# Optimization experiments

Hardware: AMD Instinct MI355X
Metric: run time of the kernel (lower is better)

## Reference

```python
import jax, jax.numpy as jnp
import numpy as np

N, IN_FEATS, OUT_FEATS = 8192, 512, 256


def setup_inputs() -> dict:
    key = jax.random.key(0)
    k1, k2, k3, k4 = jax.random.split(key, 4)
    feature_mat = jax.random.normal(k1, (N, IN_FEATS), dtype=jnp.float32)
    # Xavier-uniform style init for W and W2
    limW = float(np.sqrt(6.0 / (IN_FEATS + OUT_FEATS)))
    W = jax.random.uniform(k2, (IN_FEATS, OUT_FEATS), minval=-limW, maxval=limW, dtype=jnp.float32)
    limW2 = float(np.sqrt(6.0 / (2 * OUT_FEATS + 1)))
    W2 = jax.random.uniform(k3, (2 * OUT_FEATS, 1), minval=-limW2, maxval=limW2, dtype=jnp.float32)
    adj_mat = jax.random.randint(k4, (N, N), 0, 2, dtype=jnp.int32)
    return {"feature_mat": feature_mat, "W": W, "W2": W2, "adj_mat": adj_mat}


def reference(feature_mat, W, W2, adj_mat):
    out_feats = W.shape[1]
    Wh = feature_mat @ W                      # [N, F']
    Wh1 = Wh @ W2[:out_feats, :]              # [N, 1]
    Wh2 = Wh @ W2[out_feats:, :]              # [N, 1]
    e = Wh1 + Wh2.T                           # [N, N] broadcast add
    e = jnp.where(e > 0, e, 0.2 * e)          # leaky_relu(0.2)
    # NOTE: original masks with ZERO (not -inf) before softmax — faithful.
    e = jnp.where(adj_mat > 0, e, jnp.zeros((), dtype=e.dtype))
    attention = jax.nn.softmax(e, axis=1)     # row softmax over all N
    h_prime = attention @ Wh                  # [N, F']
    return jax.nn.relu(h_prime)
```

## Files before the change

### kernel.cpp

```cpp
#include <hip/hip_runtime.h>
#include <cstdint>
#include <cstddef>

#define NR 8192
#define FOUT 256
#define KIN 512
#define KSPLIT 4
#define JCHUNK (NR / KSPLIT)
#define BKJ 64
#define NSTEP (JCHUNK / BKJ)
#define IROWS 128

typedef __attribute__((ext_vector_type(8))) short bf16x8;
typedef __attribute__((ext_vector_type(4))) float f32x4;

__device__ __forceinline__ unsigned f2bf(float x) {
  unsigned u = __float_as_uint(x);
  u += 0x7fffu + ((u >> 16) & 1u);
  return u >> 16;
}
__device__ __forceinline__ float bf2f(unsigned h) {
  return __uint_as_float(h << 16);
}
__device__ __forceinline__ unsigned fkey(float x) {
  unsigned u = __float_as_uint(x);
  return (u & 0x80000000u) ? ~u : (u | 0x80000000u);
}
__device__ __forceinline__ float fkey_dec(unsigned k) {
  return __uint_as_float((k & 0x80000000u) ? (k ^ 0x80000000u) : ~k);
}

#define GLDS(g, l)                                                            \
  __builtin_amdgcn_global_load_lds(                                           \
      (const __attribute__((address_space(1))) unsigned int*)(g),             \
      (__attribute__((address_space(3))) unsigned int*)(l), 16, 0, 0)

__global__ __launch_bounds__(256) void k0_prep(const float* __restrict__ W,
                                               const float* __restrict__ W2,
                                               float* __restrict__ w1,
                                               float* __restrict__ w2,
                                               char* __restrict__ WTbf,
                                               unsigned* __restrict__ maxkey) {
  if (blockIdx.x == 0 && threadIdx.x == 0) *maxkey = 0u;
  int wv = threadIdx.x >> 6, lane = threadIdx.x & 63;
  int k = blockIdx.x * 4 + wv;
  int f4 = lane * 4;
  float4 wr = *(const float4*)(W + (size_t)k * FOUT + f4);
  float4 a = *(const float4*)(W2 + f4);
  float4 b = *(const float4*)(W2 + FOUT + f4);
  float d1 = wr.x * a.x + wr.y * a.y + wr.z * a.z + wr.w * a.w;
  float d2 = wr.x * b.x + wr.y * b.y + wr.z * b.z + wr.w * b.w;
#pragma unroll
  for (int off = 32; off; off >>= 1) {
    d1 += __shfl_xor(d1, off);
    d2 += __shfl_xor(d2, off);
  }
  if (lane == 0) {
    w1[k] = d1;
    w2[k] = d2;
  }
  int kt = k >> 5, kl = k & 31;
  float wv4[4] = {wr.x, wr.y, wr.z, wr.w};
#pragma unroll
  for (int ff = 0; ff < 4; ++ff) {
    int f = f4 + ff;
    size_t addr = (size_t)kt * 16384 + (f >> 4) * 1024 +
                  (((f & 15) | (((kl >> 3) & 3) << 4)) * 16) + (kl & 7) * 2;
    *(unsigned short*)(WTbf + addr) = (unsigned short)f2bf(wv4[ff]);
  }
}

__global__ __launch_bounds__(256) void k2_fused(
    const float* __restrict__ X, const char* __restrict__ WTbf,
    const float* __restrict__ w1, const float* __restrict__ w2,
    char* __restrict__ WhTf, float* __restrict__ Wh1, float* __restrict__ Wh2,
    unsigned* __restrict__ maxkey) {
  __shared__ char smem[2 * 18432 + 4096];
  char* buf0 = smem;
  char* buf1 = smem + 18432;
  char* wlds = smem + 2 * 18432;
  int t = threadIdx.x, wv = t >> 6, lane = t & 63;
  int jb = blockIdx.x * 32;
  int jr = t >> 3, koff = (t & 7) * 4;
  int cA = (jr & 15) | (((koff >> 3) & 3) << 4);
  int swA = cA ^ (((cA >> 4) & 3) << 2);
  int aoff = (jr >> 4) * 1024 + swA * 16 + ((koff & 4) << 1);
  int slotR = lane ^ (((lane >> 4) & 3) << 2);
  const float* xrow = X + (size_t)(jb + jr) * KIN + koff;

  {
    float2 a_ = *(const float2*)(w1 + t * 2);
    float2 b_ = *(const float2*)(w2 + t * 2);
    *(float2*)(wlds + t * 8) = a_;
    *(float2*)(wlds + 2048 + t * 8) = b_;
  }
  __syncthreads();

  float4 st0, st1, st2, st3;
  float d1 = 0.f, d2 = 0.f;
  f32x4 acc[2][4];
#pragma unroll
  for (int a = 0; a < 2; ++a)
#pragma unroll
    for (int b = 0; b < 4; ++b) acc[a][b] = (f32x4){0.f, 0.f, 0.f, 0.f};

#define K2_GLB(KT, BUFW)                                                      \
  do {                                                                        \
    const char* gs_ = WTbf + ((size_t)(KT) << 14) + (wv << 12) + lane * 16;   \
    char* ld_ = (BUFW) + 2048 + (wv << 12);                                   \
    GLDS(gs_, ld_);                                                           \
    GLDS(gs_ + 1024, ld_ + 1024);                                             \
    GLDS(gs_ + 2048, ld_ + 2048);                                             \
    GLDS(gs_ + 3072, ld_ + 3072);                                             \
  } while (0)

#define K2_LDX(KT, ST) (ST) = *(const float4*)(xrow + (KT) * 32)

#define K2_AGEN(ST, BUFW, SNUM)                                               \
  do {                                                                        \
    uint2 a_;                                                                 \
    a_.x = f2bf((ST).x) | (f2bf((ST).y) << 16);                               \
    a_.y = f2bf((ST).z) | (f2bf((ST).w) << 16);                               \
    *(uint2*)((BUFW) + aoff) = a_;                                            \
    float4 wa_ = *(const float4*)(wlds + ((SNUM)*32 + koff) * 4);             \
    float4 wb_ = *(const float4*)(wlds + 2048 + ((SNUM)*32 + koff) * 4);      \
    d1 += (ST).x * wa_.x + (ST).y * wa_.y + (ST).z * wa_.z + (ST).w * wa_.w;  \
    d2 += (ST).x * wb_.x + (ST).y * wb_.y + (ST).z * wb_.z + (ST).w * wb_.w;  \
  } while (0)

#define K2_ITER(S, BUFR, BUFW, STC, STF)                                      \
  do {                                                                        \
    int s_ = (S);                                                             \
    if (s_ + 1 < 16) K2_GLB(s_ + 1, BUFW);                                    \
    K2_LDX((s_ + 3 < 16) ? s_ + 3 : 15, STF);                                 \
    if (s_ + 1 < 16) K2_AGEN(STC, BUFW, s_ + 1);                              \
    bf16x8 a0 = *(const bf16x8*)((BUFR) + slotR * 16);                        \
    bf16x8 a1 = *(const bf16x8*)((BUFR) + 1024 + slotR * 16);                 \
    bf16x8 b0 = *(const bf16x8*)((BUFR) + 2048 + (wv * 4 + 0) * 1024 + lane * 16); \
    bf16x8 b1 = *(const bf16x8*)((BUFR) + 2048 + (wv * 4 + 1) * 1024 + lane * 16); \
    bf16x8 b2 = *(const bf16x8*)((BUFR) + 2048 + (wv * 4 + 2) * 1024 + lane * 16); \
    bf16x8 b3 = *(const bf16x8*)((BUFR) + 2048 + (wv * 4 + 3) * 1024 + lane * 16); \
    acc[0][0] = __builtin_amdgcn_mfma_f32_16x16x32_bf16(a0, b0, acc[0][0], 0, 0, 0); \
    acc[0][1] = __builtin_amdgcn_mfma_f32_16x16x32_bf16(a0, b1, acc[0][1], 0, 0, 0); \
    acc[0][2] = __builtin_amdgcn_mfma_f32_16x16x32_bf16(a0, b2, acc[0][2], 0, 0, 0); \
    acc[0][3] = __builtin_amdgcn_mfma_f32_16x16x32_bf16(a0, b3, acc[0][3], 0, 0, 0); \
    acc[1][0] = __builtin_amdgcn_mfma_f32_16x16x32_bf16(a1, b0, acc[1][0], 0, 0, 0); \
    acc[1][1] = __builtin_amdgcn_mfma_f32_16x16x32_bf16(a1, b1, acc[1][1], 0, 0, 0); \
    acc[1][2] = __builtin_amdgcn_mfma_f32_16x16x32_bf16(a1, b2, acc[1][2], 0, 0, 0); \
    acc[1][3] = __builtin_amdgcn_mfma_f32_16x16x32_bf16(a1, b3, acc[1][3], 0, 0, 0); \
    __builtin_amdgcn_sched_barrier(0);                                        \
    asm volatile("s_waitcnt vmcnt(1)");                                       \
    asm volatile("s_waitcnt lgkmcnt(0)");                                     \
    __builtin_amdgcn_s_barrier();                                             \
    __builtin_amdgcn_sched_barrier(0);                                        \
  } while (0)

  K2_GLB(0, buf0);
  K2_LDX(0, st0);
  K2_LDX(1, st1);
  K2_LDX(2, st2);
  K2_AGEN(st0, buf0, 0);
  __builtin_amdgcn_sched_barrier(0);
  asm volatile("s_waitcnt vmcnt(2)");
  asm volatile("s_waitcnt lgkmcnt(0)");
  __builtin_amdgcn_s_barrier();
  __builtin_amdgcn_sched_barrier(0);

  for (int s4 = 0; s4 < 16; s4 += 4) {
    K2_ITER(s4 + 0, buf0, buf1, st1, st3);
    K2_ITER(s4 + 1, buf1, buf0, st2, st0);
    K2_ITER(s4 + 2, buf0, buf1, st3, st1);
    K2_ITER(s4 + 3, buf1, buf0, st0, st2);
  }
#undef K2_ITER
#undef K2_AGEN
#undef K2_LDX
#undef K2_GLB

  int q = lane >> 4;
#pragma unroll
  for (int mi = 0; mi < 2; ++mi)
#pragma unroll
    for (int nn = 0; nn < 4; ++nn) {
      int u2 = wv * 4 + nn;
      int cell = (lane & 15) | ((((mi * 2) + (q >> 1)) & 3) << 4);
      uint2 v;
      v.x = f2bf(acc[mi][nn].x) | (f2bf(acc[mi][nn].y) << 16);
      v.y = f2bf(acc[mi][nn].z) | (f2bf(acc[mi][nn].w) << 16);
      *(uint2*)(buf0 + 2048 + u2 * 1024 + cell * 16 + ((q & 1) << 3)) = v;
    }
  __syncthreads();
  char* wb = WhTf + (size_t)blockIdx.x * 16384;
#pragma unroll
  for (int q2 = 0; q2 < 4; ++q2) {
    uint4 v = *(const uint4*)(buf0 + 2048 + q2 * 4096 + t * 16);
    *(uint4*)(wb + q2 * 4096 + t * 16) = v;
  }

  d1 += __shfl_xor(d1, 1);
  d1 += __shfl_xor(d1, 2);
  d1 += __shfl_xor(d1, 4);
  d2 += __shfl_xor(d2, 1);
  d2 += __shfl_xor(d2, 2);
  d2 += __shfl_xor(d2, 4);
  if ((t & 7) == 0) {
    Wh1[jb + jr] = d1;
    Wh2[jb + jr] = d2;
  }
  float mx = d2;
#pragma unroll
  for (int off = 32; off >= 8; off >>= 1) mx = fmaxf(mx, __shfl_xor(mx, off));
  __shared__ float red[4];
  if (lane == 0) red[wv] = mx;
  __syncthreads();
  if (t == 0) {
    float bm = fmaxf(fmaxf(red[0], red[1]), fmaxf(red[2], red[3]));
    atomicMax(maxkey, fkey(bm));
  }
}

__device__ __forceinline__ uint2 hv4(int4 aq, float4 wq, float wh1, float m,
                                     float enm, float& z) {
  float s0 = wh1 + wq.x, s1 = wh1 + wq.y, s2 = wh1 + wq.z, s3 = wh1 + wq.w;
  s0 = s0 > 0.f ? s0 : 0.2f * s0;
  s1 = s1 > 0.f ? s1 : 0.2f * s1;
  s2 = s2 > 0.f ? s2 : 0.2f * s2;
  s3 = s3 > 0.f ? s3 : 0.2f * s3;
  float w0 = aq.x > 0 ? __expf(s0 - m) : enm;
  float w1 = aq.y > 0 ? __expf(s1 - m) : enm;
  float w2 = aq.z > 0 ? __expf(s2 - m) : enm;
  float w3 = aq.w > 0 ? __expf(s3 - m) : enm;
  unsigned h0 = f2bf(w0), h1 = f2bf(w1), h2 = f2bf(w2), h3 = f2bf(w3);
  z += bf2f(h0) + bf2f(h1) + bf2f(h2) + bf2f(h3);
  uint2 r;
  r.x = h0 | (h1 << 16);
  r.y = h2 | (h3 << 16);
  return r;
}
__device__ __forceinline__ uint4 hv8(int4 a0, int4 a1, float4 w0, float4 w1,
                                     float wh1, float m, float enm, float& z) {
  uint2 r0 = hv4(a0, w0, wh1, m, enm, z);
  uint2 r1 = hv4(a1, w1, wh1, m, enm, z);
  return (uint4){r0.x, r0.y, r1.x, r1.y};
}

__global__ __launch_bounds__(1024, 4) void k3_attn(
    const int* __restrict__ adj, const char* __restrict__ WhTf,
    const float* __restrict__ Wh1, const float* __restrict__ Wh2,
    const unsigned* __restrict__ maxptr, float* __restrict__ PVp,
    float* __restrict__ Zp) {
  __shared__ char smem[40960];
  char* abuf0 = smem;
  char* abuf1 = smem + 16384;
  char* wlds = smem + 32768;
  int t = threadIdx.x, wv = t >> 6, lane = t & 63;
  int kc = blockIdx.x & 3;
  int ib = blockIdx.x >> 2;
  int ibase = ib * IROWS;
  int jbch = kc * JCHUNK;
  int r0 = t >> 3;
  int j8 = (t & 7) * 8;
  int iglob = ibase + r0;
  float maxwh2 = fkey_dec(*maxptr);
  float wh1 = Wh1[iglob];
  float m = fmaxf(0.f, wh1 + maxwh2);
  float enm = __expf(-m);
  int unitA = (r0 >> 4) * 2 + (j8 >> 5);
  int cA = (r0 & 15) | (((j8 & 31) >> 3) << 4);
  int swA = cA ^ (((cA >> 4) & 3) << 2);
  int aoff = unitA * 1024 + swA * 16;
  int slotR = lane ^ (((lane >> 4) & 3) << 2);
  const int* adjrow = adj + ((size_t)iglob << 13) + jbch + j8;
  const char* bbase = WhTf + ((size_t)(kc * 64) << 14) + (size_t)wv * 1024 +
                      (size_t)lane * 16;
  const char* wl = wlds + j8 * 4;

  *(float2*)(wlds + t * 8) = *(const float2*)(Wh2 + jbch + t * 2);
  __syncthreads();

  bf16x8 bA0, bA1, bB0, bB1;
  int4 st0_a, st0_b, st1_a, st1_b;
  f32x4 acc[8];
#pragma unroll
  for (int a = 0; a < 8; ++a) acc[a] = (f32x4){0.f, 0.f, 0.f, 0.f};
  float zacc = 0.f;

#define K3_LDB(S, B0, B1)                                                     \
  do {                                                                        \
    int sc_ = (S) < NSTEP ? (S) : NSTEP - 1;                                  \
    const char* bp_ = bbase + (size_t)(2 * sc_) * 16384;                      \
    B0 = *(const bf16x8*)(bp_);                                               \
    B1 = *(const bf16x8*)(bp_ + 16384);                                       \
  } while (0)

#define K3_LDA(S, ST)                                                         \
  do {                                                                        \
    int sc_ = (S) < NSTEP ? (S) : NSTEP - 1;                                  \
    ST##_a = *(const int4*)(adjrow + sc_ * BKJ);                              \
    ST##_b = *(const int4*)(adjrow + sc_ * BKJ + 4);                          \
  } while (0)

#define K3_ITER(S, AR, AW, BC0, BC1, BF0, BF1, STC, DO_HV)                    \
  do {                                                                        \
    int s_ = (S);                                                             \
    K3_LDB(s_ + 1, BF0, BF1);                                                 \
    if (DO_HV) {                                                              \
      float4 wq0_ = *(const float4*)(wl + (s_ + 1) * 256);                    \
      float4 wq1_ = *(const float4*)(wl + (s_ + 1) * 256 + 16);               \
      uint4 a_ = hv8(STC##_a, STC##_b, wq0_, wq1_, wh1, m, enm, zacc);        \
      *(uint4*)((AW) + aoff) = a_;                                            \
    }                                                                         \
    K3_LDA(s_ + 3, STC);                                                      \
    _Pragma("unroll")                                                         \
    for (int rf_ = 0; rf_ < 8; ++rf_) {                                       \
      bf16x8 ak0_ = *(const bf16x8*)((AR) + (rf_ * 2 + 0) * 1024 + slotR * 16); \
      bf16x8 ak1_ = *(const bf16x8*)((AR) + (rf_ * 2 + 1) * 1024 + slotR * 16); \
      acc[rf_] = __builtin_amdgcn_mfma_f32_16x16x32_bf16(ak0_, BC0, acc[rf_], 0, 0, 0); \
      acc[rf_] = __builtin_amdgcn_mfma_f32_16x16x32_bf16(ak1_, BC1, acc[rf_], 0, 0, 0); \
    }                                                                         \
    __builtin_amdgcn_sched_barrier(0);                                        \
    asm volatile("s_waitcnt lgkmcnt(0)" ::: "memory");                        \
    __builtin_amdgcn_s_barrier();                                             \
    __builtin_amdgcn_sched_barrier(0);                                        \
  } while (0)

  K3_LDB(0, bA0, bA1);
  int4 adj0a = *(const int4*)(adjrow);
  int4 adj0b = *(const int4*)(adjrow + 4);
  K3_LDA(1, st1);
  K3_LDA(2, st0);
  {
    float4 wq0 = *(const float4*)(wl);
    float4 wq1 = *(const float4*)(wl + 16);
    uint4 a0 = hv8(adj0a, adj0b, wq0, wq1, wh1, m, enm, zacc);
    *(uint4*)(abuf0 + aoff) = a0;
  }
  __builtin_amdgcn_sched_barrier(0);
  asm volatile("s_waitcnt lgkmcnt(0)" ::: "memory");
  __builtin_amdgcn_s_barrier();
  __builtin_amdgcn_sched_barrier(0);

  for (int s2 = 0; s2 < NSTEP - 2; s2 += 2) {
    K3_ITER(s2 + 0, abuf0, abuf1, bA0, bA1, bB0, bB1, st1, 1);
    K3_ITER(s2 + 1, abuf1, abuf0, bB0, bB1, bA0, bA1, st0, 1);
  }
  K3_ITER(NSTEP - 2, abuf0, abuf1, bA0, bA1, bB0, bB1, st1, 1);
  K3_ITER(NSTEP - 1, abuf1, abuf0, bB0, bB1, bA0, bA1, st0, 0);
#undef K3_ITER
#undef K3_LDA
#undef K3_LDB

  zacc += __shfl_xor(zacc, 1);
  zacc += __shfl_xor(zacc, 2);
  zacc += __shfl_xor(zacc, 4);
  if ((t & 7) == 0) Zp[(size_t)kc * NR + iglob] = zacc;
#pragma unroll
  for (int rf = 0; rf < 8; ++rf) {
    int f = wv * 16 + (lane & 15);
    int row0 = ibase + rf * 16 + ((lane >> 4) << 2);
    size_t base = ((size_t)kc * NR + row0) * FOUT + f;
    PVp[base + 0 * FOUT] = acc[rf].x;
    PVp[base + 1 * FOUT] = acc[rf].y;
    PVp[base + 2 * FOUT] = acc[rf].z;
    PVp[base + 3 * FOUT] = acc[rf].w;
  }
}

__global__ __launch_bounds__(256) void k4_reduce(const float* __restrict__ PVp,
                                                 const float* __restrict__ Zp,
                                                 float* __restrict__ out) {
  int tid = blockIdx.x * 256 + threadIdx.x;
  int i = tid >> 6;
  int f4 = (tid & 63) * 4;
  float z = Zp[i] + Zp[NR + i] + Zp[2 * NR + i] + Zp[3 * NR + i];
  float4 a = {0.f, 0.f, 0.f, 0.f};
#pragma unroll
  for (int c = 0; c < KSPLIT; ++c) {
    float4 p = *(const float4*)(PVp + ((size_t)c * NR + i) * FOUT + f4);
    a.x += p.x;
    a.y += p.y;
    a.z += p.z;
    a.w += p.w;
  }
  float inv = 1.f / z;
  float4 r;
  r.x = fmaxf(a.x * inv, 0.f);
  r.y = fmaxf(a.y * inv, 0.f);
  r.z = fmaxf(a.z * inv, 0.f);
  r.w = fmaxf(a.w * inv, 0.f);
  *(float4*)(out + (size_t)i * FOUT + f4) = r;
}

extern "C" void kernel_launch(void* const* d_in, const int* in_sizes, int n_in,
                              void* d_out, int out_size, void* d_ws,
                              size_t ws_size, hipStream_t stream) {
  const float* X = (const float*)d_in[0];
  const float* W = (const float*)d_in[1];
  const float* W2 = (const float*)d_in[2];
  const int* adj = (const int*)d_in[3];
  float* out = (float*)d_out;
  char* ws = (char*)d_ws;

  const size_t WHT_OFF = 0;
  const size_t WTBF_OFF = (size_t)4 * 1024 * 1024;
  const size_t W1_OFF = WTBF_OFF + 256 * 1024;
  const size_t W2V_OFF = W1_OFF + 2048;
  const size_t WH1_OFF = W2V_OFF + 2048;
  const size_t WH2_OFF = WH1_OFF + 32768;
  const size_t MXK_OFF = WH2_OFF + 32768;
  const size_t ZP_OFF = MXK_OFF + 256;
  const size_t PV_OFF = ZP_OFF + (size_t)KSPLIT * NR * 4;

  char* WhTf = ws + WHT_OFF;
  char* WTbf = ws + WTBF_OFF;
  float* w1 = (float*)(ws + W1_OFF);
  float* w2 = (float*)(ws + W2V_OFF);
  float* Wh1 = (float*)(ws + WH1_OFF);
  float* Wh2 = (float*)(ws + WH2_OFF);
  unsigned* maxkey = (unsigned*)(ws + MXK_OFF);
  float* Zp = (float*)(ws + ZP_OFF);
  float* PVp = (float*)(ws + PV_OFF);

  k0_prep<<<128, 256, 0, stream>>>(W, W2, w1, w2, WTbf, maxkey);
  k2_fused<<<256, 256, 0, stream>>>(X, WTbf, w1, w2, WhTf, Wh1, Wh2, maxkey);
  k3_attn<<<256, 1024, 0, stream>>>(adj, WhTf, Wh1, Wh2, maxkey, PVp, Zp);
  k4_reduce<<<2048, 256, 0, stream>>>(PVp, Zp, out);
}
```

Baseline: 113.0 us.

## Pack adjacency matrix into bitmap before attention kernel

Adds a pre-pass kernel that converts the int32 adjacency matrix into a 1-bit-per-entry bitmap, and makes the attention kernel read one mask byte per 8 columns instead of two int4 loads. The intent is to shrink the attention kernel's global traffic and register pressure so it becomes MFMA-bound. The full adjacency is still streamed once by the new pack kernel, adding a launch and a workspace round-trip. The leaky-relu is also rewritten branchlessly with fmaxf.

```diff
diff --git a/kernel.cpp b/kernel.cpp
--- a/kernel.cpp
+++ b/kernel.cpp
@@ -34,6 +34,26 @@
   __builtin_amdgcn_global_load_lds(                                           \
       (const __attribute__((address_space(1))) unsigned int*)(g),             \
       (__attribute__((address_space(3))) unsigned int*)(l), 16, 0, 0)
+
+__global__ __launch_bounds__(256) void k_pack(const int* __restrict__ adj,
+                                              unsigned* __restrict__ bmp) {
+  int t = threadIdx.x, lane = t & 63;
+  size_t waveId = (size_t)blockIdx.x * 4 + (t >> 6);
+  size_t base = waveId * 8192;
+  const int* p = adj + base + (size_t)lane * 4;
+  unsigned* wp = bmp + base / 32 + (lane >> 3);
+  bool wr = (lane & 7) == 0;
+#pragma unroll 4
+  for (int s = 0; s < 32; ++s) {
+    int4 v = *(const int4*)(p + s * 256);
+    unsigned nib = (v.x > 0 ? 1u : 0u) | (v.y > 0 ? 2u : 0u) |
+                   (v.z > 0 ? 4u : 0u) | (v.w > 0 ? 8u : 0u);
+    unsigned b1 = nib | (((unsigned)__shfl_xor((int)nib, 1)) << 4);
+    unsigned b2 = b1 | (((unsigned)__shfl_xor((int)b1, 2)) << 8);
+    unsigned b3 = b2 | (((unsigned)__shfl_xor((int)b2, 4)) << 16);
+    if (wr) wp[s * 8] = b3;
+  }
+}
 
 __global__ __launch_bounds__(256) void k0_prep(const float* __restrict__ W,
                                                const float* __restrict__ W2,
@@ -219,33 +239,36 @@
   }
 }
 
-__device__ __forceinline__ uint2 hv4(int4 aq, float4 wq, float wh1, float m,
-                                     float enm, float& z) {
-  float s0 = wh1 + wq.x, s1 = wh1 + wq.y, s2 = wh1 + wq.z, s3 = wh1 + wq.w;
-  s0 = s0 > 0.f ? s0 : 0.2f * s0;
-  s1 = s1 > 0.f ? s1 : 0.2f * s1;
-  s2 = s2 > 0.f ? s2 : 0.2f * s2;
-  s3 = s3 > 0.f ? s3 : 0.2f * s3;
-  float w0 = aq.x > 0 ? __expf(s0 - m) : enm;
-  float w1 = aq.y > 0 ? __expf(s1 - m) : enm;
-  float w2 = aq.z > 0 ? __expf(s2 - m) : enm;
-  float w3 = aq.w > 0 ? __expf(s3 - m) : enm;
-  unsigned h0 = f2bf(w0), h1 = f2bf(w1), h2 = f2bf(w2), h3 = f2bf(w3);
-  z += bf2f(h0) + bf2f(h1) + bf2f(h2) + bf2f(h3);
-  uint2 r;
-  r.x = h0 | (h1 << 16);
-  r.y = h2 | (h3 << 16);
-  return r;
-}
-__device__ __forceinline__ uint4 hv8(int4 a0, int4 a1, float4 w0, float4 w1,
-                                     float wh1, float m, float enm, float& z) {
-  uint2 r0 = hv4(a0, w0, wh1, m, enm, z);
-  uint2 r1 = hv4(a1, w1, wh1, m, enm, z);
-  return (uint4){r0.x, r0.y, r1.x, r1.y};
+__device__ __forceinline__ uint4 hv8m(unsigned mb, float4 w0, float4 w1,
+                                      float wh1, float m, float enm, float& z) {
+  float s0 = wh1 + w0.x, s1 = wh1 + w0.y, s2 = wh1 + w0.z, s3 = wh1 + w0.w;
+  float s4 = wh1 + w1.x, s5 = wh1 + w1.y, s6 = wh1 + w1.z, s7 = wh1 + w1.w;
+  s0 = fmaxf(s0, 0.2f * s0);
+  s1 = fmaxf(s1, 0.2f * s1);
+  s2 = fmaxf(s2, 0.2f * s2);
+  s3 = fmaxf(s3, 0.2f * s3);
+  s4 = fmaxf(s4, 0.2f * s4);
+  s5 = fmaxf(s5, 0.2f * s5);
+  s6 = fmaxf(s6, 0.2f * s6);
+  s7 = fmaxf(s7, 0.2f * s7);
+  float e0 = (mb & 1u) ? __expf(s0 - m) : enm;
+  float e1 = (mb & 2u) ? __expf(s1 - m) : enm;
+  float e2 = (mb & 4u) ? __expf(s2 - m) : enm;
+  float e3 = (mb & 8u) ? __expf(s3 - m) : enm;
+  float e4 = (mb & 16u) ? __expf(s4 - m) : enm;
+  float e5 = (mb & 32u) ? __expf(s5 - m) : enm;
+  float e6 = (mb & 64u) ? __expf(s6 - m) : enm;
+  float e7 = (mb & 128u) ? __expf(s7 - m) : enm;
+  unsigned h0 = f2bf(e0), h1 = f2bf(e1), h2 = f2bf(e2), h3 = f2bf(e3);
+  unsigned h4 = f2bf(e4), h5 = f2bf(e5), h6 = f2bf(e6), h7 = f2bf(e7);
+  z += bf2f(h0) + bf2f(h1) + bf2f(h2) + bf2f(h3) + bf2f(h4) + bf2f(h5) +
+       bf2f(h6) + bf2f(h7);
+  return (uint4){h0 | (h1 << 16), h2 | (h3 << 16), h4 | (h5 << 16),
+                 h6 | (h7 << 16)};
 }
 
 __global__ __launch_bounds__(1024, 4) void k3_attn(
-    const int* __restrict__ adj, const char* __restrict__ WhTf,
+    const unsigned char* __restrict__ bmp, const char* __restrict__ WhTf,
     const float* __restrict__ Wh1, const float* __restrict__ Wh2,
     const unsigned* __restrict__ maxptr, float* __restrict__ PVp,
     float* __restrict__ Zp) {
@@ -270,7 +293,8 @@
   int swA = cA ^ (((cA >> 4) & 3) << 2);
   int aoff = unitA * 1024 + swA * 16;
   int slotR = lane ^ (((lane >> 4) & 3) << 2);
-  const int* adjrow = adj + ((size_t)iglob << 13) + jbch + j8;
+  const unsigned char* mrow = bmp + (size_t)iglob * (NR / 8) + (jbch >> 3) +
+                              (t & 7);
   const char* bbase = WhTf + ((size_t)(kc * 64) << 14) + (size_t)wv * 1024 +
                       (size_t)lane * 16;
   const char* wl = wlds + j8 * 4;
@@ -279,7 +303,7 @@
   __syncthreads();
 
   bf16x8 bA0, bA1, bB0, bB1;
-  int4 st0_a, st0_b, st1_a, st1_b;
+  unsigned st0, st1;
   f32x4 acc[8];
 #pragma unroll
   for (int a = 0; a < 8; ++a) acc[a] = (f32x4){0.f, 0.f, 0.f, 0.f};
@@ -293,11 +317,10 @@
     B1 = *(const bf16x8*)(bp_ + 16384);                                       \
   } while (0)
 
-#define K3_LDA(S, ST)                                                         \
+#define K3_LDM(S, ST)                                                         \
   do {                                                                        \
     int sc_ = (S) < NSTEP ? (S) : NSTEP - 1;                                  \
-    ST##_a = *(const int4*)(adjrow + sc_ * BKJ);                              \
-    ST##_b = *(const int4*)(adjrow + sc_ * BKJ + 4);                          \
+    ST = (unsigned)mrow[sc_ * 8];                                             \
   } while (0)
 
 #define K3_ITER(S, AR, AW, BC0, BC1, BF0, BF1, STC, DO_HV)                    \
@@ -307,10 +330,10 @@
     if (DO_HV) {                                                              \
       float4 wq0_ = *(const float4*)(wl + (s_ + 1) * 256);                    \
       float4 wq1_ = *(const float4*)(wl + (s_ + 1) * 256 + 16);               \
-      uint4 a_ = hv8(STC##_a, STC##_b, wq0_, wq1_, wh1, m, enm, zacc);        \
+      uint4 a_ = hv8m(STC, wq0_, wq1_, wh1, m, enm, zacc);                    \
       *(uint4*)((AW) + aoff) = a_;                                            \
     }                                                                         \
-    K3_LDA(s_ + 3, STC);                                                      \
+    K3_LDM(s_ + 3, STC);                                                      \
     _Pragma("unroll")                                                         \
     for (int rf_ = 0; rf_ < 8; ++rf_) {                                       \
       bf16x8 ak0_ = *(const bf16x8*)((AR) + (rf_ * 2 + 0) * 1024 + slotR * 16); \
@@ -325,14 +348,13 @@
   } while (0)
 
   K3_LDB(0, bA0, bA1);
-  int4 adj0a = *(const int4*)(adjrow);
-  int4 adj0b = *(const int4*)(adjrow + 4);
-  K3_LDA(1, st1);
-  K3_LDA(2, st0);
+  unsigned mb0 = (unsigned)mrow[0];
+  K3_LDM(1, st1);
+  K3_LDM(2, st0);
   {
     float4 wq0 = *(const float4*)(wl);
     float4 wq1 = *(const float4*)(wl + 16);
-    uint4 a0 = hv8(adj0a, adj0b, wq0, wq1, wh1, m, enm, zacc);
+    uint4 a0 = hv8m(mb0, wq0, wq1, wh1, m, enm, zacc);
     *(uint4*)(abuf0 + aoff) = a0;
   }
   __builtin_amdgcn_sched_barrier(0);
@@ -347,7 +369,7 @@
   K3_ITER(NSTEP - 2, abuf0, abuf1, bA0, bA1, bB0, bB1, st1, 1);
   K3_ITER(NSTEP - 1, abuf1, abuf0, bB0, bB1, bA0, bA1, st0, 0);
 #undef K3_ITER
-#undef K3_LDA
+#undef K3_LDM
 #undef K3_LDB
 
   zacc += __shfl_xor(zacc, 1);
@@ -410,6 +432,7 @@
   const size_t MXK_OFF = WH2_OFF + 32768;
   const size_t ZP_OFF = MXK_OFF + 256;
   const size_t PV_OFF = ZP_OFF + (size_t)KSPLIT * NR * 4;
+  const size_t BMP_OFF = PV_OFF + (size_t)KSPLIT * NR * FOUT * 4;
 
   char* WhTf = ws + WHT_OFF;
   char* WTbf = ws + WTBF_OFF;
@@ -420,9 +443,12 @@
   unsigned* maxkey = (unsigned*)(ws + MXK_OFF);
   float* Zp = (float*)(ws + ZP_OFF);
   float* PVp = (float*)(ws + PV_OFF);
-
+  unsigned* bmp = (unsigned*)(ws + BMP_OFF);
+
+  k_pack<<<2048, 256, 0, stream>>>(adj, bmp);
   k0_prep<<<128, 256, 0, stream>>>(W, W2, w1, w2, WTbf, maxkey);
   k2_fused<<<256, 256, 0, stream>>>(X, WTbf, w1, w2, WhTf, Wh1, Wh2, maxkey);
-  k3_attn<<<256, 1024, 0, stream>>>(adj, WhTf, Wh1, Wh2, maxkey, PVp, Zp);
+  k3_attn<<<256, 1024, 0, stream>>>((const unsigned char*)bmp, WhTf, Wh1, Wh2,
+                                    maxkey, PVp, Zp);
   k4_reduce<<<2048, 256, 0, stream>>>(PVp, Zp, out);
 }
```

New measurement: 141.7 us. 25.4% more time.
